# Kernel optimization log

Hardware: AMD Instinct MI355X
Metric: run time of the kernel (lower is better)

Reference implementation:

```python
import jax, jax.numpy as jnp
import numpy as np

LN_EPS = 1e-5


def _layer_norm(x, w, b, eps=LN_EPS):
    mu = jnp.mean(x, axis=-1, keepdims=True)
    var = jnp.var(x, axis=-1, keepdims=True)
    return (x - mu) * jax.lax.rsqrt(var + eps) * w + b


def setup_inputs() -> dict:
    key = jax.random.key(0)
    ks = jax.random.split(key, 6)
    H, I, B, S = 1024, 4096, 4, 2048
    return {
        "x": jax.random.normal(ks[0], (B, S, H), jnp.float32),
        "ln_weight": jnp.ones((H,), jnp.float32),
        "ln_bias": jnp.zeros((H,), jnp.float32),
        "i2h_weight": jax.random.normal(ks[1], (2 * I, H), jnp.float32) * 0.02,
        "i2h_bias": jax.random.normal(ks[2], (2 * I,), jnp.float32) * 0.02,
        "h2o_weight": jax.random.normal(ks[3], (H, I), jnp.float32) * 0.02,
        "h2o_bias": jax.random.normal(ks[4], (H,), jnp.float32) * 0.02,
        "post_ln_weight": jnp.ones((H,), jnp.float32),
        "post_ln_bias": jnp.zeros((H,), jnp.float32),
    }


def reference(x, ln_weight, ln_bias, i2h_weight, i2h_bias, h2o_weight, h2o_bias,
              post_ln_weight, post_ln_bias):
    B, S, H = x.shape
    x2 = x.reshape(-1, H)  # [N, H]
    x_ln = _layer_norm(x2, ln_weight, ln_bias)
    # i2h: [N, 2I]
    pre = jnp.einsum('nh,oh->no', x_ln, i2h_weight) + i2h_bias
    I = pre.shape[-1] // 2
    pre_gate, lin = pre[:, :I], pre[:, I:]
    # gated gelu (tanh-approx, matching gelu_fused)
    hid = jax.nn.gelu(pre_gate, approximate=True) * lin
    out = jnp.einsum('ni,oi->no', hid, h2o_weight) + h2o_bias
    out = _layer_norm(out, post_ln_weight, post_ln_bias)
    out = out + x2  # residual (dropout=0)
    return out.reshape(B, S, H)
```

## Files before the change

kernel.cpp:

```cpp
#include <hip/hip_runtime.h>
#include <stdint.h>

#define N_ROWS 8192
#define H_DIM  1024
#define I_DIM  4096

typedef unsigned short u16;
typedef __bf16 bf16x8 __attribute__((ext_vector_type(8)));
typedef float f32x4 __attribute__((ext_vector_type(4)));
typedef u16 u16x4 __attribute__((ext_vector_type(4)));

#define BAR()   asm volatile("s_barrier" ::: "memory")
#define LGKM0() asm volatile("s_waitcnt lgkmcnt(0)" ::: "memory")
#define VMW(n)  asm volatile("s_waitcnt vmcnt(" #n ")" ::: "memory")

__device__ __forceinline__ u16 f2bf(float f) {
    union { float f; uint32_t u; } v; v.f = f;
    uint32_t u = v.u;
    u += 0x7FFFu + ((u >> 16) & 1u);
    return (u16)(u >> 16);
}

__device__ __forceinline__ float bf2f(u16 h) {
    union { uint32_t u; float f; } v; v.u = ((uint32_t)h) << 16;
    return v.f;
}

__device__ __forceinline__ float gelu_tanh(float x) {
    float u = 0.7978845608028654f * (x + 0.044715f * x * x * x);
    u = fminf(fmaxf(u, -15.f), 15.f);
    float e = __expf(2.f * u);
    float t = (e - 1.f) / (e + 1.f);
    return 0.5f * x * (1.f + t);
}

__device__ __forceinline__ void load_lds16(const void* g, void* l) {
    auto gp = reinterpret_cast<const __attribute__((address_space(1))) uint32_t*>(
        reinterpret_cast<uintptr_t>(g));
    auto lp = reinterpret_cast<__attribute__((address_space(3))) uint32_t*>(
        static_cast<uint32_t>(reinterpret_cast<uintptr_t>(l)));
    __builtin_amdgcn_global_load_lds(gp, lp, 16, 0, 0);
}

__global__ __launch_bounds__(512, 2) void gemm1_gated(
    const u16* __restrict__ A, const u16* __restrict__ W,
    const float* __restrict__ bias, u16* __restrict__ hid)
{
    __shared__ u16 lds[2 * 32768];
    const int t = threadIdx.x;
    const int lane = t & 63, wid = t >> 6;
    const int wm = wid >> 2, wn = wid & 3;
    const int g = lane >> 4, r16 = lane & 15;

    const int brow = blockIdx.y * 256;
    const int bcol = blockIdx.x * 128;

    const int tr = t >> 2;
    const int swz8 = ((t & 3) ^ ((tr >> 1) & 3)) * 8;
    const u16* pA = A + (size_t)(brow + tr) * H_DIM + swz8;
    const int j0 = tr, j1 = tr + 128;
    const int c0 = bcol + ((j0 >> 6) << 5) + (j0 & 31);
    const int c1 = bcol + ((j1 >> 6) << 5) + (j1 & 31);
    const u16* pB0 = W + (size_t)(((j0 & 63) < 32) ? c0 : (I_DIM + c0)) * H_DIM + swz8;
    const u16* pB1 = W + (size_t)(((j1 & 63) < 32) ? c1 : (I_DIM + c1)) * H_DIM + swz8;
    const int dst = t * 8;

    const int sl  = (g ^ ((r16 >> 1) & 3)) * 8;
    const int rdA = (wm * 128 + r16) * 32 + sl;
    const int rdB = 16384 + (wn * 64 + r16) * 32 + sl;

    f32x4 acc[8][4] = {};

    u16* const B0 = lds;
    u16* const B1 = lds + 32768;

#define STG_A1(S, kk, ks) do { \
    load_lds16(pA + (kk) + (ks) * 32,                       (S) + (ks) * 8192 + dst); \
    load_lds16(pA + (size_t)128 * H_DIM + (kk) + (ks) * 32, (S) + (ks) * 8192 + 4096 + dst); } while (0)
#define STG_B1(S, kk, ks) do { \
    load_lds16(pB0 + (kk) + (ks) * 32, (S) + 16384 + (ks) * 8192 + dst); \
    load_lds16(pB1 + (kk) + (ks) * 32, (S) + 16384 + (ks) * 8192 + 4096 + dst); } while (0)
#define RD_A1(L, ks, mh) { _Pragma("unroll") for (int m = 0; m < 4; ++m) \
    af[m] = *(const bf16x8*)((L) + (ks) * 8192 + rdA + ((mh) * 4 + m) * 512); }
#define RD_B1(L, ks) { _Pragma("unroll") for (int n = 0; n < 4; ++n) \
    bf[n] = *(const bf16x8*)((L) + (ks) * 8192 + rdB + n * 512); }
#define MM1(mh) { _Pragma("unroll") for (int m = 0; m < 4; ++m) _Pragma("unroll") for (int n = 0; n < 4; ++n) \
    acc[(mh) * 4 + m][n] = __builtin_amdgcn_mfma_f32_16x16x32_bf16(af[m], bf[n], acc[(mh) * 4 + m][n], 0, 0, 0); }

    STG_A1(B0, 0, 0); STG_B1(B0, 0, 0);
    STG_A1(B0, 0, 1); STG_B1(B0, 0, 1);
    STG_A1(B1, 64, 0); STG_B1(B1, 64, 0);
    VMW(4); BAR();

    const int NI = H_DIM / 128;
#pragma unroll 1
    for (int it = 0; it < NI; ++it) {
        const int kk1 = (2 * it + 1) * 64;
        const int kk2 = (2 * it + 2) * 64;
        const int kk3 = (2 * it + 3) * 64;
        const bool s2 = (it + 1 < NI);
        const bool last = (it == NI - 1);
        bf16x8 af[4], bf[4];

        STG_A1(B1, kk1, 1); STG_B1(B1, kk1, 1);
        RD_A1(B0, 0, 0); RD_B1(B0, 0);
        BAR(); LGKM0();
        __builtin_amdgcn_s_setprio(1); MM1(0); __builtin_amdgcn_s_setprio(0);
        BAR();

        if (s2) STG_B1(B0, kk2, 0);
        RD_A1(B0, 0, 1);
        BAR(); LGKM0();
        __builtin_amdgcn_s_setprio(1); MM1(1); __builtin_amdgcn_s_setprio(0);
        BAR();

        if (s2) STG_A1(B0, kk2, 0);
        RD_A1(B0, 1, 0); RD_B1(B0, 1);
        BAR(); LGKM0();
        __builtin_amdgcn_s_setprio(1); MM1(0); __builtin_amdgcn_s_setprio(0);
        BAR();

        if (s2) STG_B1(B0, kk2, 1);
        RD_A1(B0, 1, 1);
        BAR(); LGKM0();
        __builtin_amdgcn_s_setprio(1); MM1(1); __builtin_amdgcn_s_setprio(0);
        if (last) { VMW(0); } else { VMW(6); }
        BAR();

        if (s2) STG_A1(B0, kk2, 1);
        RD_A1(B1, 0, 0); RD_B1(B1, 0);
        BAR(); LGKM0();
        __builtin_amdgcn_s_setprio(1); MM1(0); __builtin_amdgcn_s_setprio(0);
        BAR();

        if (s2) STG_B1(B1, kk3, 0);
        RD_A1(B1, 0, 1);
        BAR(); LGKM0();
        __builtin_amdgcn_s_setprio(1); MM1(1); __builtin_amdgcn_s_setprio(0);
        BAR();

        if (s2) STG_A1(B1, kk3, 0);
        RD_A1(B1, 1, 0); RD_B1(B1, 1);
        BAR(); LGKM0();
        __builtin_amdgcn_s_setprio(1); MM1(0); __builtin_amdgcn_s_setprio(0);
        BAR();

        RD_A1(B1, 1, 1);
        BAR(); LGKM0();
        __builtin_amdgcn_s_setprio(1); MM1(1); __builtin_amdgcn_s_setprio(0);
        if (last) { VMW(0); } else { VMW(4); }
        BAR();
    }
#undef STG_A1
#undef STG_B1
#undef RD_A1
#undef RD_B1
#undef MM1

#pragma unroll
    for (int n = 0; n < 2; ++n) {
        const int cg = bcol + wn * 32 + n * 16 + r16;
        const float bgv = bias[cg], blv = bias[I_DIM + cg];
#pragma unroll
        for (int m = 0; m < 8; ++m) {
            const int row = brow + wm * 128 + m * 16 + g * 4;
            u16* hp = hid + (size_t)row * I_DIM + cg;
#pragma unroll
            for (int r = 0; r < 4; ++r) {
                float gate = acc[m][n][r] + bgv;
                float lin  = acc[m][n + 2][r] + blv;
                hp[(size_t)r * I_DIM] = f2bf(gelu_tanh(gate) * lin);
            }
        }
    }
}

__global__ __launch_bounds__(512, 2) void gemm2_k(
    const u16* __restrict__ A, const u16* __restrict__ W,
    const float* __restrict__ bias, u16* __restrict__ opb)
{
    __shared__ u16 lds[2 * 24576];
    const int t = threadIdx.x;
    const int lane = t & 63, wid = t >> 6;
    const int wm = wid >> 1, wn = wid & 1;
    const int g = lane >> 4, r16 = lane & 15;

    const int brow = blockIdx.y * 256;
    const int bcol = blockIdx.x * 128;

    const int tr = t >> 2;
    const int swz8 = ((t & 3) ^ ((tr >> 1) & 3)) * 8;
    const u16* pA = A + (size_t)(brow + tr) * I_DIM + swz8;
    const u16* pB = W + (size_t)(bcol + tr) * I_DIM + swz8;
    const int dst = t * 8;

    const int sl  = (g ^ ((r16 >> 1) & 3)) * 8;
    const int rdA = (wm * 64 + r16) * 32 + sl;
    const int rdB = 16384 + (wn * 64 + r16) * 32 + sl;

    f32x4 acc[4][4] = {};

    u16* const B0 = lds;
    u16* const B1 = lds + 24576;

#define STG_A2(S, kk, ks) do { \
    load_lds16(pA + (kk) + (ks) * 32,                       (S) + (ks) * 8192 + dst); \
    load_lds16(pA + (size_t)128 * I_DIM + (kk) + (ks) * 32, (S) + (ks) * 8192 + 4096 + dst); } while (0)
#define STG_B2(S, kk, ks) do { \
    load_lds16(pB + (kk) + (ks) * 32, (S) + 16384 + (ks) * 4096 + dst); } while (0)
#define RD_A2(L, ks, mh) { _Pragma("unroll") for (int m = 0; m < 2; ++m) \
    af[m] = *(const bf16x8*)((L) + (ks) * 8192 + rdA + ((mh) * 2 + m) * 512); }
#define RD_B2(L, ks) { _Pragma("unroll") for (int n = 0; n < 4; ++n) \
    bf[n] = *(const bf16x8*)((L) + (ks) * 4096 + rdB + n * 512); }
#define MM2(mh) { _Pragma("unroll") for (int m = 0; m < 2; ++m) _Pragma("unroll") for (int n = 0; n < 4; ++n) \
    acc[(mh) * 2 + m][n] = __builtin_amdgcn_mfma_f32_16x16x32_bf16(af[m], bf[n], acc[(mh) * 2 + m][n], 0, 0, 0); }

    STG_A2(B0, 0, 0); STG_B2(B0, 0, 0);
    STG_A2(B0, 0, 1); STG_B2(B0, 0, 1);
    STG_A2(B1, 64, 0); STG_B2(B1, 64, 0);
    VMW(3); BAR();

    const int NI = I_DIM / 128;
#pragma unroll 1
    for (int it = 0; it < NI; ++it) {
        const int kk1 = (2 * it + 1) * 64;
        const int kk2 = (2 * it + 2) * 64;
        const int kk3 = (2 * it + 3) * 64;
        const bool s2 = (it + 1 < NI);
        const bool last = (it == NI - 1);
        bf16x8 af[2], bf[4];

        STG_A2(B1, kk1, 1); STG_B2(B1, kk1, 1);
        RD_A2(B0, 0, 0); RD_B2(B0, 0);
        BAR(); LGKM0();
        __builtin_amdgcn_s_setprio(1); MM2(0); __builtin_amdgcn_s_setprio(0);
        BAR();

        if (s2) STG_B2(B0, kk2, 0);
        RD_A2(B0, 0, 1);
        BAR(); LGKM0();
        __builtin_amdgcn_s_setprio(1); MM2(1); __builtin_amdgcn_s_setprio(0);
        BAR();

        if (s2) STG_A2(B0, kk2, 0);
        RD_A2(B0, 1, 0); RD_B2(B0, 1);
        BAR(); LGKM0();
        __builtin_amdgcn_s_setprio(1); MM2(0); __builtin_amdgcn_s_setprio(0);
        BAR();

        if (s2) STG_B2(B0, kk2, 1);
        RD_A2(B0, 1, 1);
        BAR(); LGKM0();
        __builtin_amdgcn_s_setprio(1); MM2(1); __builtin_amdgcn_s_setprio(0);
        if (last) { VMW(0); } else { VMW(4); }
        BAR();

        if (s2) STG_A2(B0, kk2, 1);
        RD_A2(B1, 0, 0); RD_B2(B1, 0);
        BAR(); LGKM0();
        __builtin_amdgcn_s_setprio(1); MM2(0); __builtin_amdgcn_s_setprio(0);
        BAR();

        if (s2) STG_B2(B1, kk3, 0);
        RD_A2(B1, 0, 1);
        BAR(); LGKM0();
        __builtin_amdgcn_s_setprio(1); MM2(1); __builtin_amdgcn_s_setprio(0);
        BAR();

        if (s2) STG_A2(B1, kk3, 0);
        RD_A2(B1, 1, 0); RD_B2(B1, 1);
        BAR(); LGKM0();
        __builtin_amdgcn_s_setprio(1); MM2(0); __builtin_amdgcn_s_setprio(0);
        BAR();

        RD_A2(B1, 1, 1);
        BAR(); LGKM0();
        __builtin_amdgcn_s_setprio(1); MM2(1); __builtin_amdgcn_s_setprio(0);
        if (last) { VMW(0); } else { VMW(3); }
        BAR();
    }
#undef STG_A2
#undef STG_B2
#undef RD_A2
#undef RD_B2
#undef MM2

#pragma unroll
    for (int n = 0; n < 4; ++n) {
        const int cg = bcol + wn * 64 + n * 16 + r16;
        const float bv = bias[cg];
#pragma unroll
        for (int m = 0; m < 4; ++m) {
            const int row = brow + wm * 64 + m * 16 + g * 4;
            u16* op = opb + (size_t)row * H_DIM + cg;
#pragma unroll
            for (int r = 0; r < 4; ++r)
                op[(size_t)r * H_DIM] = f2bf(acc[m][n][r] + bv);
        }
    }
}

__device__ __forceinline__ void block_mean_var(float s, float s2, float* red, int t,
                                               float& mu, float& var) {
#pragma unroll
    for (int off = 32; off > 0; off >>= 1) {
        s  += __shfl_down(s, off);
        s2 += __shfl_down(s2, off);
    }
    const int wid = t >> 6;
    if ((t & 63) == 0) { red[wid] = s; red[4 + wid] = s2; }
    __syncthreads();
    if (t == 0) {
        float a = red[0] + red[1] + red[2] + red[3];
        float b = red[4] + red[5] + red[6] + red[7];
        red[0] = a * (1.f / H_DIM);
        red[1] = b * (1.f / H_DIM);
    }
    __syncthreads();
    mu = red[0];
    var = red[1] - mu * mu;
}

__global__ void ln_pre(const float* __restrict__ x, const float* __restrict__ w,
                       const float* __restrict__ b, u16* __restrict__ xln)
{
    __shared__ float red[8];
    const int row = blockIdx.x, t = threadIdx.x;
    const float4 v = reinterpret_cast<const float4*>(x + (size_t)row * H_DIM)[t];
    float mu, var;
    block_mean_var(v.x + v.y + v.z + v.w,
                   v.x * v.x + v.y * v.y + v.z * v.z + v.w * v.w, red, t, mu, var);
    const float rstd = rsqrtf(var + 1e-5f);
    const float4 wv = reinterpret_cast<const float4*>(w)[t];
    const float4 bv = reinterpret_cast<const float4*>(b)[t];
    u16x4 o;
    o.x = f2bf((v.x - mu) * rstd * wv.x + bv.x);
    o.y = f2bf((v.y - mu) * rstd * wv.y + bv.y);
    o.z = f2bf((v.z - mu) * rstd * wv.z + bv.z);
    o.w = f2bf((v.w - mu) * rstd * wv.w + bv.w);
    reinterpret_cast<u16x4*>(xln + (size_t)row * H_DIM)[t] = o;
}

__global__ void ln_post_res(const u16* __restrict__ op, const float* __restrict__ w,
                            const float* __restrict__ b, const float* __restrict__ x,
                            float* __restrict__ out)
{
    __shared__ float red[8];
    const int row = blockIdx.x, t = threadIdx.x;
    const u16x4 hv = reinterpret_cast<const u16x4*>(op + (size_t)row * H_DIM)[t];
    float4 v;
    v.x = bf2f(hv.x); v.y = bf2f(hv.y); v.z = bf2f(hv.z); v.w = bf2f(hv.w);
    float mu, var;
    block_mean_var(v.x + v.y + v.z + v.w,
                   v.x * v.x + v.y * v.y + v.z * v.z + v.w * v.w, red, t, mu, var);
    const float rstd = rsqrtf(var + 1e-5f);
    const float4 wv = reinterpret_cast<const float4*>(w)[t];
    const float4 bv = reinterpret_cast<const float4*>(b)[t];
    const float4 xv = reinterpret_cast<const float4*>(x + (size_t)row * H_DIM)[t];
    float4 o;
    o.x = (v.x - mu) * rstd * wv.x + bv.x + xv.x;
    o.y = (v.y - mu) * rstd * wv.y + bv.y + xv.y;
    o.z = (v.z - mu) * rstd * wv.z + bv.z + xv.z;
    o.w = (v.w - mu) * rstd * wv.w + bv.w + xv.w;
    reinterpret_cast<float4*>(out + (size_t)row * H_DIM)[t] = o;
}

__global__ void cvt_bf16(const float* __restrict__ in, u16* __restrict__ out, int n4) {
    int i = blockIdx.x * blockDim.x + threadIdx.x;
    if (i >= n4) return;
    float4 v = reinterpret_cast<const float4*>(in)[i];
    u16x4 o = { f2bf(v.x), f2bf(v.y), f2bf(v.z), f2bf(v.w) };
    reinterpret_cast<u16x4*>(out)[i] = o;
}

extern "C" void kernel_launch(void* const* d_in, const int* in_sizes, int n_in,
                              void* d_out, int out_size, void* d_ws, size_t ws_size,
                              hipStream_t stream)
{
    const float* x   = (const float*)d_in[0];
    const float* lnw = (const float*)d_in[1];
    const float* lnb = (const float*)d_in[2];
    const float* w1  = (const float*)d_in[3];
    const float* b1  = (const float*)d_in[4];
    const float* w2  = (const float*)d_in[5];
    const float* b2  = (const float*)d_in[6];
    const float* pw  = (const float*)d_in[7];
    const float* pb  = (const float*)d_in[8];
    float* out = (float*)d_out;

    char* ws = (char*)d_ws;
    u16* xln = (u16*)(ws);
    u16* w1b = (u16*)(ws + (16u << 20));
    u16* hid = (u16*)(ws + (32u << 20));
    u16* w2b = (u16*)(ws);
    u16* opb = (u16*)(ws + (8u << 20));

    cvt_bf16<<<(2 * I_DIM * H_DIM / 4 + 255) / 256, 256, 0, stream>>>(w1, w1b, 2 * I_DIM * H_DIM / 4);
    ln_pre<<<N_ROWS, 256, 0, stream>>>(x, lnw, lnb, xln);
    gemm1_gated<<<dim3(I_DIM / 128, N_ROWS / 256), 512, 0, stream>>>(xln, w1b, b1, hid);
    cvt_bf16<<<(H_DIM * I_DIM / 4 + 255) / 256, 256, 0, stream>>>(w2, w2b, H_DIM * I_DIM / 4);
    gemm2_k<<<dim3(H_DIM / 128, N_ROWS / 256), 512, 0, stream>>>(hid, w2b, b2, opb);
    ln_post_res<<<N_ROWS, 256, 0, stream>>>(opb, pw, pb, x, out);
}
```

Measured before the change: 270.7 us.

## Loop gemm1 blocks over four column tiles, widen gemm2 steps, merge prep kernels

gemm1 now has each block walk four 128-column tiles serially, with the gated-GELU epilogue running every eight iterations, so the grid shrinks to 8x32 blocks. gemm2 restructures its pipeline into four larger phases with 4x4 MFMA groups per read, which means fewer barriers. The layernorm and both weight conversions are merged into one prep launch, and the workspace layout changes to match. The smaller gemm1 grid of 256 blocks risks lower occupancy and parallelism in exchange for better A-tile reuse in L2.

```diff
diff --git a/kernel.cpp b/kernel.cpp
--- a/kernel.cpp
+++ b/kernel.cpp
@@ -52,15 +52,15 @@
     const int wm = wid >> 2, wn = wid & 3;
     const int g = lane >> 4, r16 = lane & 15;
 
-    const int brow = blockIdx.y * 256;
-    const int bcol = blockIdx.x * 128;
+    const int brow  = blockIdx.y * 256;
+    const int bcol0 = blockIdx.x * 512;
 
     const int tr = t >> 2;
     const int swz8 = ((t & 3) ^ ((tr >> 1) & 3)) * 8;
     const u16* pA = A + (size_t)(brow + tr) * H_DIM + swz8;
     const int j0 = tr, j1 = tr + 128;
-    const int c0 = bcol + ((j0 >> 6) << 5) + (j0 & 31);
-    const int c1 = bcol + ((j1 >> 6) << 5) + (j1 & 31);
+    const int c0 = bcol0 + ((j0 >> 6) << 5) + (j0 & 31);
+    const int c1 = bcol0 + ((j1 >> 6) << 5) + (j1 & 31);
     const u16* pB0 = W + (size_t)(((j0 & 63) < 32) ? c0 : (I_DIM + c0)) * H_DIM + swz8;
     const u16* pB1 = W + (size_t)(((j1 & 63) < 32) ? c1 : (I_DIM + c1)) * H_DIM + swz8;
     const int dst = t * 8;
@@ -74,12 +74,14 @@
     u16* const B0 = lds;
     u16* const B1 = lds + 32768;
 
-#define STG_A1(S, kk, ks) do { \
-    load_lds16(pA + (kk) + (ks) * 32,                       (S) + (ks) * 8192 + dst); \
-    load_lds16(pA + (size_t)128 * H_DIM + (kk) + (ks) * 32, (S) + (ks) * 8192 + 4096 + dst); } while (0)
-#define STG_B1(S, kk, ks) do { \
-    load_lds16(pB0 + (kk) + (ks) * 32, (S) + 16384 + (ks) * 8192 + dst); \
-    load_lds16(pB1 + (kk) + (ks) * 32, (S) + 16384 + (ks) * 8192 + 4096 + dst); } while (0)
+#define AOFF(n) (((n) & 15) * 64)
+#define BOFF(n) ((size_t)((n) >> 4) * (128 * H_DIM) + (size_t)(((n) & 15) * 64))
+#define STG_A1(S, ao, ks) do { \
+    load_lds16(pA + (ao) + (ks) * 32,                       (S) + (ks) * 8192 + dst); \
+    load_lds16(pA + (size_t)128 * H_DIM + (ao) + (ks) * 32, (S) + (ks) * 8192 + 4096 + dst); } while (0)
+#define STG_B1(S, bo, ks) do { \
+    load_lds16(pB0 + (bo) + (ks) * 32, (S) + 16384 + (ks) * 8192 + dst); \
+    load_lds16(pB1 + (bo) + (ks) * 32, (S) + 16384 + (ks) * 8192 + 4096 + dst); } while (0)
 #define RD_A1(L, ks, mh) { _Pragma("unroll") for (int m = 0; m < 4; ++m) \
     af[m] = *(const bf16x8*)((L) + (ks) * 8192 + rdA + ((mh) * 4 + m) * 512); }
 #define RD_B1(L, ks) { _Pragma("unroll") for (int n = 0; n < 4; ++n) \
@@ -87,59 +89,59 @@
 #define MM1(mh) { _Pragma("unroll") for (int m = 0; m < 4; ++m) _Pragma("unroll") for (int n = 0; n < 4; ++n) \
     acc[(mh) * 4 + m][n] = __builtin_amdgcn_mfma_f32_16x16x32_bf16(af[m], bf[n], acc[(mh) * 4 + m][n], 0, 0, 0); }
 
-    STG_A1(B0, 0, 0); STG_B1(B0, 0, 0);
-    STG_A1(B0, 0, 1); STG_B1(B0, 0, 1);
-    STG_A1(B1, 64, 0); STG_B1(B1, 64, 0);
+    STG_A1(B0, 0, 0); STG_B1(B0, (size_t)0, 0);
+    STG_A1(B0, 0, 1); STG_B1(B0, (size_t)0, 1);
+    STG_A1(B1, AOFF(1), 0); STG_B1(B1, BOFF(1), 0);
     VMW(4); BAR();
 
-    const int NI = H_DIM / 128;
+    const int NI = 32;
 #pragma unroll 1
     for (int it = 0; it < NI; ++it) {
-        const int kk1 = (2 * it + 1) * 64;
-        const int kk2 = (2 * it + 2) * 64;
-        const int kk3 = (2 * it + 3) * 64;
+        const int nO = 2 * it + 1, nE2 = 2 * it + 2, nO2 = 2 * it + 3;
+        const int    aO = AOFF(nO), aE2 = AOFF(nE2), aO2 = AOFF(nO2);
+        const size_t bO = BOFF(nO), bE2 = BOFF(nE2), bO2 = BOFF(nO2);
         const bool s2 = (it + 1 < NI);
         const bool last = (it == NI - 1);
         bf16x8 af[4], bf[4];
 
-        STG_A1(B1, kk1, 1); STG_B1(B1, kk1, 1);
+        STG_A1(B1, aO, 1); STG_B1(B1, bO, 1);
         RD_A1(B0, 0, 0); RD_B1(B0, 0);
         BAR(); LGKM0();
         __builtin_amdgcn_s_setprio(1); MM1(0); __builtin_amdgcn_s_setprio(0);
         BAR();
 
-        if (s2) STG_B1(B0, kk2, 0);
+        if (s2) STG_B1(B0, bE2, 0);
         RD_A1(B0, 0, 1);
         BAR(); LGKM0();
         __builtin_amdgcn_s_setprio(1); MM1(1); __builtin_amdgcn_s_setprio(0);
         BAR();
 
-        if (s2) STG_A1(B0, kk2, 0);
+        if (s2) STG_A1(B0, aE2, 0);
         RD_A1(B0, 1, 0); RD_B1(B0, 1);
         BAR(); LGKM0();
         __builtin_amdgcn_s_setprio(1); MM1(0); __builtin_amdgcn_s_setprio(0);
         BAR();
 
-        if (s2) STG_B1(B0, kk2, 1);
+        if (s2) STG_B1(B0, bE2, 1);
         RD_A1(B0, 1, 1);
         BAR(); LGKM0();
         __builtin_amdgcn_s_setprio(1); MM1(1); __builtin_amdgcn_s_setprio(0);
         if (last) { VMW(0); } else { VMW(6); }
         BAR();
 
-        if (s2) STG_A1(B0, kk2, 1);
+        if (s2) STG_A1(B0, aE2, 1);
         RD_A1(B1, 0, 0); RD_B1(B1, 0);
         BAR(); LGKM0();
         __builtin_amdgcn_s_setprio(1); MM1(0); __builtin_amdgcn_s_setprio(0);
         BAR();
 
-        if (s2) STG_B1(B1, kk3, 0);
+        if (s2) STG_B1(B1, bO2, 0);
         RD_A1(B1, 0, 1);
         BAR(); LGKM0();
         __builtin_amdgcn_s_setprio(1); MM1(1); __builtin_amdgcn_s_setprio(0);
         BAR();
 
-        if (s2) STG_A1(B1, kk3, 0);
+        if (s2) STG_A1(B1, aO2, 0);
         RD_A1(B1, 1, 0); RD_B1(B1, 1);
         BAR(); LGKM0();
         __builtin_amdgcn_s_setprio(1); MM1(0); __builtin_amdgcn_s_setprio(0);
@@ -150,29 +152,36 @@
         __builtin_amdgcn_s_setprio(1); MM1(1); __builtin_amdgcn_s_setprio(0);
         if (last) { VMW(0); } else { VMW(4); }
         BAR();
-    }
+
+        if ((it & 7) == 7) {
+            const int ct = it >> 3;
+#pragma unroll
+            for (int n = 0; n < 2; ++n) {
+                const int cg = bcol0 + ct * 128 + wn * 32 + n * 16 + r16;
+                const float bgv = bias[cg], blv = bias[I_DIM + cg];
+#pragma unroll
+                for (int m = 0; m < 8; ++m) {
+                    const int row = brow + wm * 128 + m * 16 + g * 4;
+                    u16* hp = hid + (size_t)row * I_DIM + cg;
+#pragma unroll
+                    for (int r = 0; r < 4; ++r) {
+                        float gate = acc[m][n][r] + bgv;
+                        float lin  = acc[m][n + 2][r] + blv;
+                        hp[(size_t)r * I_DIM] = f2bf(gelu_tanh(gate) * lin);
+                        acc[m][n][r] = 0.f;
+                        acc[m][n + 2][r] = 0.f;
+                    }
+                }
+            }
+        }
+    }
+#undef AOFF
+#undef BOFF
 #undef STG_A1
 #undef STG_B1
 #undef RD_A1
 #undef RD_B1
 #undef MM1
-
-#pragma unroll
-    for (int n = 0; n < 2; ++n) {
-        const int cg = bcol + wn * 32 + n * 16 + r16;
-        const float bgv = bias[cg], blv = bias[I_DIM + cg];
-#pragma unroll
-        for (int m = 0; m < 8; ++m) {
-            const int row = brow + wm * 128 + m * 16 + g * 4;
-            u16* hp = hid + (size_t)row * I_DIM + cg;
-#pragma unroll
-            for (int r = 0; r < 4; ++r) {
-                float gate = acc[m][n][r] + bgv;
-                float lin  = acc[m][n + 2][r] + blv;
-                hp[(size_t)r * I_DIM] = f2bf(gelu_tanh(gate) * lin);
-            }
-        }
-    }
 }
 
 __global__ __launch_bounds__(512, 2) void gemm2_k(
@@ -208,81 +217,59 @@
     load_lds16(pA + (size_t)128 * I_DIM + (kk) + (ks) * 32, (S) + (ks) * 8192 + 4096 + dst); } while (0)
 #define STG_B2(S, kk, ks) do { \
     load_lds16(pB + (kk) + (ks) * 32, (S) + 16384 + (ks) * 4096 + dst); } while (0)
-#define RD_A2(L, ks, mh) { _Pragma("unroll") for (int m = 0; m < 2; ++m) \
-    af[m] = *(const bf16x8*)((L) + (ks) * 8192 + rdA + ((mh) * 2 + m) * 512); }
-#define RD_B2(L, ks) { _Pragma("unroll") for (int n = 0; n < 4; ++n) \
+#define RD2(L, ks) { _Pragma("unroll") for (int m = 0; m < 4; ++m) \
+    af[m] = *(const bf16x8*)((L) + (ks) * 8192 + rdA + m * 512); \
+    _Pragma("unroll") for (int n = 0; n < 4; ++n) \
     bf[n] = *(const bf16x8*)((L) + (ks) * 4096 + rdB + n * 512); }
-#define MM2(mh) { _Pragma("unroll") for (int m = 0; m < 2; ++m) _Pragma("unroll") for (int n = 0; n < 4; ++n) \
-    acc[(mh) * 2 + m][n] = __builtin_amdgcn_mfma_f32_16x16x32_bf16(af[m], bf[n], acc[(mh) * 2 + m][n], 0, 0, 0); }
+#define MM2() { _Pragma("unroll") for (int m = 0; m < 4; ++m) _Pragma("unroll") for (int n = 0; n < 4; ++n) \
+    acc[m][n] = __builtin_amdgcn_mfma_f32_16x16x32_bf16(af[m], bf[n], acc[m][n], 0, 0, 0); }
 
     STG_A2(B0, 0, 0); STG_B2(B0, 0, 0);
     STG_A2(B0, 0, 1); STG_B2(B0, 0, 1);
     STG_A2(B1, 64, 0); STG_B2(B1, 64, 0);
-    VMW(3); BAR();
+    VMW(6); BAR();
 
     const int NI = I_DIM / 128;
 #pragma unroll 1
     for (int it = 0; it < NI; ++it) {
-        const int kk1 = (2 * it + 1) * 64;
-        const int kk2 = (2 * it + 2) * 64;
-        const int kk3 = (2 * it + 3) * 64;
+        const int kkO  = (2 * it + 1) * 64;
+        const int kkE2 = (2 * it + 2) * 64;
+        const int kkO2 = (2 * it + 3) * 64;
         const bool s2 = (it + 1 < NI);
         const bool last = (it == NI - 1);
-        bf16x8 af[2], bf[4];
-
-        STG_A2(B1, kk1, 1); STG_B2(B1, kk1, 1);
-        RD_A2(B0, 0, 0); RD_B2(B0, 0);
-        BAR(); LGKM0();
-        __builtin_amdgcn_s_setprio(1); MM2(0); __builtin_amdgcn_s_setprio(0);
-        BAR();
-
-        if (s2) STG_B2(B0, kk2, 0);
-        RD_A2(B0, 0, 1);
-        BAR(); LGKM0();
-        __builtin_amdgcn_s_setprio(1); MM2(1); __builtin_amdgcn_s_setprio(0);
-        BAR();
-
-        if (s2) STG_A2(B0, kk2, 0);
-        RD_A2(B0, 1, 0); RD_B2(B0, 1);
-        BAR(); LGKM0();
-        __builtin_amdgcn_s_setprio(1); MM2(0); __builtin_amdgcn_s_setprio(0);
-        BAR();
-
-        if (s2) STG_B2(B0, kk2, 1);
-        RD_A2(B0, 1, 1);
-        BAR(); LGKM0();
-        __builtin_amdgcn_s_setprio(1); MM2(1); __builtin_amdgcn_s_setprio(0);
-        if (last) { VMW(0); } else { VMW(4); }
-        BAR();
-
-        if (s2) STG_A2(B0, kk2, 1);
-        RD_A2(B1, 0, 0); RD_B2(B1, 0);
-        BAR(); LGKM0();
-        __builtin_amdgcn_s_setprio(1); MM2(0); __builtin_amdgcn_s_setprio(0);
-        BAR();
-
-        if (s2) STG_B2(B1, kk3, 0);
-        RD_A2(B1, 0, 1);
-        BAR(); LGKM0();
-        __builtin_amdgcn_s_setprio(1); MM2(1); __builtin_amdgcn_s_setprio(0);
-        BAR();
-
-        if (s2) STG_A2(B1, kk3, 0);
-        RD_A2(B1, 1, 0); RD_B2(B1, 1);
-        BAR(); LGKM0();
-        __builtin_amdgcn_s_setprio(1); MM2(0); __builtin_amdgcn_s_setprio(0);
-        BAR();
-
-        RD_A2(B1, 1, 1);
-        BAR(); LGKM0();
-        __builtin_amdgcn_s_setprio(1); MM2(1); __builtin_amdgcn_s_setprio(0);
-        if (last) { VMW(0); } else { VMW(3); }
+        bf16x8 af[4], bf[4];
+
+        STG_A2(B1, kkO, 1); STG_B2(B1, kkO, 1);
+        RD2(B0, 0);
+        BAR(); LGKM0();
+        __builtin_amdgcn_s_setprio(1); MM2(); __builtin_amdgcn_s_setprio(0);
+        VMW(6);
+        BAR();
+
+        if (s2) { STG_A2(B0, kkE2, 0); STG_B2(B0, kkE2, 0); }
+        RD2(B0, 1);
+        BAR(); LGKM0();
+        __builtin_amdgcn_s_setprio(1); MM2(); __builtin_amdgcn_s_setprio(0);
+        if (last) { VMW(3); } else { VMW(6); }
+        BAR();
+
+        if (s2) { STG_A2(B0, kkE2, 1); STG_B2(B0, kkE2, 1); }
+        RD2(B1, 0);
+        BAR(); LGKM0();
+        __builtin_amdgcn_s_setprio(1); MM2(); __builtin_amdgcn_s_setprio(0);
+        if (last) { VMW(0); } else { VMW(6); }
+        BAR();
+
+        if (s2) { STG_A2(B1, kkO2, 0); STG_B2(B1, kkO2, 0); }
+        RD2(B1, 1);
+        BAR(); LGKM0();
+        __builtin_amdgcn_s_setprio(1); MM2(); __builtin_amdgcn_s_setprio(0);
+        if (!last) { VMW(6); }
         BAR();
     }
 #undef STG_A2
 #undef STG_B2
-#undef RD_A2
-#undef RD_B2
+#undef RD2
 #undef MM2
 
 #pragma unroll
@@ -321,24 +308,39 @@
     var = red[1] - mu * mu;
 }
 
-__global__ void ln_pre(const float* __restrict__ x, const float* __restrict__ w,
-                       const float* __restrict__ b, u16* __restrict__ xln)
+__global__ __launch_bounds__(256) void prep(
+    const float* __restrict__ x, const float* __restrict__ lnw,
+    const float* __restrict__ lnb, u16* __restrict__ xln,
+    const float* __restrict__ w1, u16* __restrict__ w1b,
+    const float* __restrict__ w2, u16* __restrict__ w2b)
 {
     __shared__ float red[8];
-    const int row = blockIdx.x, t = threadIdx.x;
-    const float4 v = reinterpret_cast<const float4*>(x + (size_t)row * H_DIM)[t];
-    float mu, var;
-    block_mean_var(v.x + v.y + v.z + v.w,
-                   v.x * v.x + v.y * v.y + v.z * v.z + v.w * v.w, red, t, mu, var);
-    const float rstd = rsqrtf(var + 1e-5f);
-    const float4 wv = reinterpret_cast<const float4*>(w)[t];
-    const float4 bv = reinterpret_cast<const float4*>(b)[t];
-    u16x4 o;
-    o.x = f2bf((v.x - mu) * rstd * wv.x + bv.x);
-    o.y = f2bf((v.y - mu) * rstd * wv.y + bv.y);
-    o.z = f2bf((v.z - mu) * rstd * wv.z + bv.z);
-    o.w = f2bf((v.w - mu) * rstd * wv.w + bv.w);
-    reinterpret_cast<u16x4*>(xln + (size_t)row * H_DIM)[t] = o;
+    const int bid = blockIdx.x, t = threadIdx.x;
+    if (bid < N_ROWS) {
+        const float4 v = reinterpret_cast<const float4*>(x + (size_t)bid * H_DIM)[t];
+        float mu, var;
+        block_mean_var(v.x + v.y + v.z + v.w,
+                       v.x * v.x + v.y * v.y + v.z * v.z + v.w * v.w, red, t, mu, var);
+        const float rstd = rsqrtf(var + 1e-5f);
+        const float4 wv = reinterpret_cast<const float4*>(lnw)[t];
+        const float4 bv = reinterpret_cast<const float4*>(lnb)[t];
+        u16x4 o;
+        o.x = f2bf((v.x - mu) * rstd * wv.x + bv.x);
+        o.y = f2bf((v.y - mu) * rstd * wv.y + bv.y);
+        o.z = f2bf((v.z - mu) * rstd * wv.z + bv.z);
+        o.w = f2bf((v.w - mu) * rstd * wv.w + bv.w);
+        reinterpret_cast<u16x4*>(xln + (size_t)bid * H_DIM)[t] = o;
+    } else if (bid < N_ROWS + 8192) {
+        const int i = (bid - N_ROWS) * 256 + t;
+        const float4 v = reinterpret_cast<const float4*>(w1)[i];
+        u16x4 o = { f2bf(v.x), f2bf(v.y), f2bf(v.z), f2bf(v.w) };
+        reinterpret_cast<u16x4*>(w1b)[i] = o;
+    } else {
+        const int i = (bid - N_ROWS - 8192) * 256 + t;
+        const float4 v = reinterpret_cast<const float4*>(w2)[i];
+        u16x4 o = { f2bf(v.x), f2bf(v.y), f2bf(v.z), f2bf(v.w) };
+        reinterpret_cast<u16x4*>(w2b)[i] = o;
+    }
 }
 
 __global__ void ln_post_res(const u16* __restrict__ op, const float* __restrict__ w,
@@ -365,14 +367,6 @@
     reinterpret_cast<float4*>(out + (size_t)row * H_DIM)[t] = o;
 }
 
-__global__ void cvt_bf16(const float* __restrict__ in, u16* __restrict__ out, int n4) {
-    int i = blockIdx.x * blockDim.x + threadIdx.x;
-    if (i >= n4) return;
-    float4 v = reinterpret_cast<const float4*>(in)[i];
-    u16x4 o = { f2bf(v.x), f2bf(v.y), f2bf(v.z), f2bf(v.w) };
-    reinterpret_cast<u16x4*>(out)[i] = o;
-}
-
 extern "C" void kernel_launch(void* const* d_in, const int* in_sizes, int n_in,
                               void* d_out, int out_size, void* d_ws, size_t ws_size,
                               hipStream_t stream)
@@ -392,13 +386,11 @@
     u16* xln = (u16*)(ws);
     u16* w1b = (u16*)(ws + (16u << 20));
     u16* hid = (u16*)(ws + (32u << 20));
-    u16* w2b = (u16*)(ws);
-    u16* opb = (u16*)(ws + (8u << 20));
-
-    cvt_bf16<<<(2 * I_DIM * H_DIM / 4 + 255) / 256, 256, 0, stream>>>(w1, w1b, 2 * I_DIM * H_DIM / 4);
-    ln_pre<<<N_ROWS, 256, 0, stream>>>(x, lnw, lnb, xln);
-    gemm1_gated<<<dim3(I_DIM / 128, N_ROWS / 256), 512, 0, stream>>>(xln, w1b, b1, hid);
-    cvt_bf16<<<(H_DIM * I_DIM / 4 + 255) / 256, 256, 0, stream>>>(w2, w2b, H_DIM * I_DIM / 4);
+    u16* w2b = (u16*)(ws + (96u << 20));
+    u16* opb = (u16*)(ws);
+
+    prep<<<20480, 256, 0, stream>>>(x, lnw, lnb, xln, w1, w1b, w2, w2b);
+    gemm1_gated<<<dim3(8, N_ROWS / 256), 512, 0, stream>>>(xln, w1b, b1, hid);
     gemm2_k<<<dim3(H_DIM / 128, N_ROWS / 256), 512, 0, stream>>>(hid, w2b, b2, opb);
     ln_post_res<<<N_ROWS, 256, 0, stream>>>(opb, pw, pb, x, out);
 }
```

New measurement: 267.5 us. About the same (-1.2%).
